# Kernel optimization log

Measured on AMD Instinct MI355X. Metric: run time of the kernel, lower is better.

## Reference

```python
import jax, jax.numpy as jnp
import numpy as np

N = 4096          # batch of candidate observations
D = 1024          # embedding dim
N_CLASSES = 100
GTG_MAX_ITER = 30 # gtg_tol=0.0 -> while loop always runs max_iter steps
PERC_LABELED = 0.5
EPS = 1e-8        # matches the +1e-08 in sum_X_A_X


def setup_inputs() -> dict:
    key = jax.random.key(0)
    k1, k2 = jax.random.split(key)
    embedding = jax.random.normal(k1, (N, D), dtype=jnp.float32)
    labels = jax.random.randint(k2, (N,), 0, N_CLASSES, dtype=jnp.int32)
    return {"embedding": embedding, "labels": labels}


def _cos_affinity(E):
    # F.normalize(E, dim=-1) with eps=1e-12, then relu(En @ En.T), diag := 1
    En = E / jnp.maximum(jnp.linalg.norm(E, axis=-1, keepdims=True), 1e-12)
    A = jax.nn.relu(En @ En.T)                      # [N, N]
    n = A.shape[0]
    idx = jnp.arange(n)
    A = A.at[idx, idx].set(1.0)
    return A, En


def reference(embedding, labels):
    n = embedding.shape[0]

    # ---- get_A_rbfk (A_function='cos_sim', rbf_aff=True) ----
    A, En = _cos_affinity(embedding)
    # 7th neighbor by descending cosine similarity (column index 6)
    idx7 = jnp.argsort(-A, axis=1)[:, 6]            # [N]
    # sigma_i = relu(cos(x_i, seventh_i)) -- the [0,1] entry of the 2x2 cos-sim matrix
    sigmas = jax.nn.relu(jnp.sum(En * En[idx7], axis=-1))  # [N]
    A = jnp.exp(-(A ** 2) / (sigmas[:, None] * sigmas[None, :]))

    # ---- threshold (strategy='mean', cos_sim branch) ----
    A = jnp.where(A < jnp.mean(A), 0.0, A)

    # ---- get_X: first n_lab indices labeled (one-hot), rest uniform 1/C ----
    n_lab = int(n * PERC_LABELED)
    labeled = jnp.arange(n) < n_lab                 # [N] bool
    one_hot = jax.nn.one_hot(labels, N_CLASSES, dtype=jnp.float32)
    X0 = jnp.where(labeled[:, None], one_hot, jnp.float32(1.0 / N_CLASSES))

    # ---- graph transduction game: X <- (X + X*(A@X)) / rowsum ----
    def step(X, _):
        mm_A_X = A @ X                              # [N, C]
        mult = X + X * mm_A_X
        Xn = mult / (jnp.sum(mult, axis=1, keepdims=True) + EPS)
        ent = -jnp.sum(Xn * jnp.log(Xn + EPS), axis=1)  # per-row entropy history
        return Xn, ent

    Xf, _ent_hist = jax.lax.scan(step, X0, None, length=GTG_MAX_ITER)
    return Xf
```

## Files before the change

### kernel.cpp

```cpp
#include <hip/hip_runtime.h>
#include <math.h>

typedef unsigned short ushortT;
typedef __attribute__((ext_vector_type(8))) short short8;
typedef __attribute__((ext_vector_type(4))) float f32x4;

#define NN 4096
#define DD 1024
#define NC 100
#define CP 128
#define NLAB 2048
#define NITER 30

__device__ __forceinline__ ushortT bf16rn(float x) {
  unsigned u = __float_as_uint(x);
  unsigned r = (u + 0x7fffu + ((u >> 16) & 1u)) >> 16;
  return (ushortT)r;
}
__device__ __forceinline__ float bf2f(ushortT h) {
  return __uint_as_float(((unsigned)h) << 16);
}
__device__ __forceinline__ void gload16(const void* g, void* l) {
  __builtin_amdgcn_global_load_lds((const __attribute__((address_space(1))) char*)g,
                                   (__attribute__((address_space(3))) char*)l, 16, 0, 0);
}

__global__ __launch_bounds__(256) void k_normalize(const float* __restrict__ E,
                                                   ushortT* __restrict__ Enh,
                                                   ushortT* __restrict__ Enl) {
  int row = blockIdx.x, t = threadIdx.x;
  const float4* e4 = (const float4*)(E + (size_t)row * DD);
  float4 v = e4[t];
  float ss = v.x * v.x + v.y * v.y + v.z * v.z + v.w * v.w;
  __shared__ float red[4];
  int lane = t & 63, w = t >> 6;
#pragma unroll
  for (int off = 32; off; off >>= 1) ss += __shfl_xor(ss, off);
  if (lane == 0) red[w] = ss;
  __syncthreads();
  float tot = red[0] + red[1] + red[2] + red[3];
  float d = fmaxf(sqrtf(tot), 1e-12f);
  float xs[4] = {v.x / d, v.y / d, v.z / d, v.w / d};
  ushort4 hv, lv;
  ushortT h;
  h = bf16rn(xs[0]); hv.x = h; lv.x = bf16rn(xs[0] - bf2f(h));
  h = bf16rn(xs[1]); hv.y = h; lv.y = bf16rn(xs[1] - bf2f(h));
  h = bf16rn(xs[2]); hv.z = h; lv.z = bf16rn(xs[2] - bf2f(h));
  h = bf16rn(xs[3]); hv.w = h; lv.w = bf16rn(xs[3] - bf2f(h));
  ((ushort4*)Enh)[(size_t)row * 256 + t] = hv;
  ((ushort4*)Enl)[(size_t)row * 256 + t] = lv;
}

__global__ __launch_bounds__(256, 4) void k_syrk_mfma(const ushortT* __restrict__ Enh,
                                                      const ushortT* __restrict__ Enl,
                                                      float* __restrict__ A) {
  int xg = (int)blockIdx.x & 7;
  int j = (int)blockIdx.x >> 3;
  int bi = -1, bj = 0;
#pragma unroll
  for (int p = 0; p < 4; ++p) {
    int bic = xg + (p << 3);
    int c = 32 - bic;
    if (bi < 0) {
      if (j < c) { bi = bic; bj = bic + j; } else j -= c;
    }
  }
  if (bi < 0) return;
  __shared__ ushortT lds[18432];
  int t = threadIdx.x;
  int l = t & 63, w = t >> 6;
  int i0 = bi << 7, j0 = bj << 7;
  int wr = w >> 1, wc = w & 1;
  f32x4 zz = {0.f, 0.f, 0.f, 0.f};
  f32x4 acc[4][4];
#pragma unroll
  for (int m = 0; m < 4; ++m)
#pragma unroll
    for (int n = 0; n < 4; ++n) acc[m][n] = zz;
  int arow_l = l & 15, kslot = l >> 4;

  for (int s = 0; s < 48; ++s) {
    int term = s >> 4;
    int kk0 = (s & 15) << 6;
    const ushortT* sa = (term == 2) ? Enl : Enh;
    const ushortT* sb = (term == 1) ? Enl : Enh;
#pragma unroll
    for (int q = 0; q < 4; ++q) {
      int n = (q << 8) + t;
      int r = n >> 3, p = n & 7;
      int col = (p ^ (r & 7)) << 3;
      gload16(sa + (size_t)(i0 + r) * DD + kk0 + col, &lds[n << 3]);
      gload16(sb + (size_t)(j0 + r) * DD + kk0 + col, &lds[8192 + (n << 3)]);
    }
    __syncthreads();
#pragma unroll
    for (int kk = 0; kk < 2; ++kk) {
      int g = (kk << 2) + kslot;
      short8 av[4], bv[4];
#pragma unroll
      for (int m = 0; m < 4; ++m) {
        int r = (wr << 6) + (m << 4) + arow_l;
        av[m] = *(const short8*)&lds[(r << 6) + ((g ^ (r & 7)) << 3)];
      }
#pragma unroll
      for (int n = 0; n < 4; ++n) {
        int r = (wc << 6) + (n << 4) + arow_l;
        bv[n] = *(const short8*)&lds[8192 + (r << 6) + ((g ^ (r & 7)) << 3)];
      }
#pragma unroll
      for (int m = 0; m < 4; ++m)
#pragma unroll
        for (int n = 0; n < 4; ++n)
          acc[m][n] = __builtin_amdgcn_mfma_f32_16x16x32_bf16(av[m], bv[n], acc[m][n], 0, 0, 0);
    }
    __syncthreads();
  }
  int rbase = (l >> 4) << 2;
#pragma unroll
  for (int m = 0; m < 4; ++m) {
#pragma unroll
    for (int n = 0; n < 4; ++n) {
#pragma unroll
      for (int r = 0; r < 4; ++r) {
        int gi = i0 + (wr << 6) + (m << 4) + rbase + r;
        int gj = j0 + (wc << 6) + (n << 4) + (l & 15);
        float v = fmaxf(acc[m][n][r], 0.0f);
        if (gi == gj) v = 1.0f;
        A[(size_t)gi * NN + gj] = v;
      }
    }
  }
  if (bi != bj) {
    float* T = (float*)&lds[0];
#pragma unroll
    for (int c2 = 0; c2 < 2; ++c2) {
      __syncthreads();
      if (wr == c2) {
#pragma unroll
        for (int m = 0; m < 4; ++m)
#pragma unroll
          for (int n = 0; n < 4; ++n)
#pragma unroll
            for (int r = 0; r < 4; ++r)
              T[(((wc << 6) + (n << 4) + (l & 15)) * 68) + (m << 4) + rbase + r] =
                  fmaxf(acc[m][n][r], 0.0f);
      }
      __syncthreads();
      int lj = t >> 1, cg = (t & 1) << 5;
#pragma unroll
      for (int q = 0; q < 8; ++q) {
        float4 vq = *(const float4*)&T[lj * 68 + cg + (q << 2)];
        *(float4*)&A[(size_t)(j0 + lj) * NN + i0 + (c2 << 6) + cg + (q << 2)] = vq;
      }
    }
  }
}

__device__ __forceinline__ void ins7(float (&tv)[7], float v) {
  if (v > tv[6]) {
#pragma unroll
    for (int s = 0; s < 7; s++) {
      if (v > tv[s]) { float tmp = tv[s]; tv[s] = v; v = tmp; }
    }
  }
}
__global__ __launch_bounds__(256) void k_top7(const float* __restrict__ A,
                                              float* __restrict__ sig) {
  int w = threadIdx.x >> 6, lane = threadIdx.x & 63;
  int row = (blockIdx.x << 2) + w;
  const float4* a4 = (const float4*)(A + (size_t)row * NN);
  float tv[7];
#pragma unroll
  for (int i = 0; i < 7; i++) tv[i] = -1.0f;
  for (int k = 0; k < 16; k++) {
    float4 v = a4[(k << 6) + lane];
    ins7(tv, v.x); ins7(tv, v.y); ins7(tv, v.z); ins7(tv, v.w);
  }
  int head = 0;
  float seventh = 0.0f;
  for (int r = 0; r < 7; r++) {
    float h = (head < 7) ? tv[head] : -1.0f;
    float m = h;
#pragma unroll
    for (int off = 32; off; off >>= 1) m = fmaxf(m, __shfl_xor(m, off));
    unsigned long long ball = __ballot(h == m);
    if (lane == (__ffsll(ball) - 1)) head++;
    seventh = m;
  }
  if (lane == 0) sig[row] = seventh;
}

__global__ __launch_bounds__(256) void k_transform(const float* __restrict__ A,
                                                   const float* __restrict__ sig,
                                                   double* __restrict__ parts) {
  int row = blockIdx.x;
  float si = sig[row];
  const float4* a4 = (const float4*)(A + (size_t)row * NN);
  const float4* s4 = (const float4*)sig;
  int t = threadIdx.x;
  double local = 0.0;
#pragma unroll
  for (int k = 0; k < 4; k++) {
    int j = (k << 8) + t;
    float4 v = a4[j];
    float4 sg = s4[j];
    local += (double)expf(-(v.x * v.x) / (si * sg.x)) +
             (double)expf(-(v.y * v.y) / (si * sg.y)) +
             (double)expf(-(v.z * v.z) / (si * sg.z)) +
             (double)expf(-(v.w * v.w) / (si * sg.w));
  }
  __shared__ double dred[4];
  int lane = t & 63, wv = t >> 6;
#pragma unroll
  for (int off = 32; off; off >>= 1) local += __shfl_xor(local, off);
  if (lane == 0) dred[wv] = local;
  __syncthreads();
  if (t == 0) parts[row] = dred[0] + dred[1] + dred[2] + dred[3];
}

__global__ __launch_bounds__(256) void k_mean(const double* __restrict__ parts,
                                              float* __restrict__ meanb) {
  int t = threadIdx.x;
  double local = 0.0;
#pragma unroll
  for (int k = 0; k < NN / 256; k++) local += parts[(k << 8) + t];
  __shared__ double dred[4];
  int lane = t & 63, wv = t >> 6;
#pragma unroll
  for (int off = 32; off; off >>= 1) local += __shfl_xor(local, off);
  if (lane == 0) dred[wv] = local;
  __syncthreads();
  if (t == 0) meanb[0] = (float)((dred[0] + dred[1] + dred[2] + dred[3]) / ((double)NN * (double)NN));
}

__global__ __launch_bounds__(256) void k_thresh_pack(const float* __restrict__ A,
                                                     const float* __restrict__ sig,
                                                     const float* __restrict__ meanb,
                                                     ushortT* __restrict__ ApL,
                                                     ushortT* __restrict__ ApU) {
  float m = meanb[0];
  int i4 = ((int)blockIdx.x << 8) + threadIdx.x;
  int row2 = i4 >> 10;
  int col4 = (i4 & 1023) << 2;
  int grow = NLAB + row2;
  float si = sig[grow];
  float4 v = *(const float4*)&A[(size_t)grow * NN + col4];
  float4 sg = *(const float4*)&sig[col4];
  float c0 = expf(-(v.x * v.x) / (si * sg.x));
  float c1 = expf(-(v.y * v.y) / (si * sg.y));
  float c2 = expf(-(v.z * v.z) / (si * sg.z));
  float c3 = expf(-(v.w * v.w) / (si * sg.w));
  c0 = (c0 < m) ? 0.0f : c0;
  c1 = (c1 < m) ? 0.0f : c1;
  c2 = (c2 < m) ? 0.0f : c2;
  c3 = (c3 < m) ? 0.0f : c3;
  int half = col4 >> 11;
  int cc = col4 & 2047;
  int rt = row2 >> 4, arow = row2 & 15;
  int kc = cc >> 5, khi = (cc >> 3) & 3, k0 = cc & 7;
  ushortT* dst = half ? ApU : ApL;
  ushort4 hv;
  hv.x = bf16rn(c0); hv.y = bf16rn(c1); hv.z = bf16rn(c2); hv.w = bf16rn(c3);
  *(ushort4*)&dst[((size_t)((rt << 6) + kc) << 9) + (khi << 7) + (arow << 3) + k0] = hv;
}

__global__ __launch_bounds__(256) void k_xlabp(const int* __restrict__ labels,
                                               ushortT* __restrict__ Xlabp) {
  int idx = ((int)blockIdx.x << 8) + threadIdx.x;
  int c = idx >> 11, j = idx & 2047;
  int kc = j >> 5, khi = (j >> 3) & 3, k0 = j & 7;
  int cf = c >> 4, slot = c & 15;
  Xlabp[((size_t)(((kc << 3) + cf) << 2) + khi) * 128 + (slot << 3) + k0] =
      (labels[j] == c) ? (ushortT)0x3F80 : (ushortT)0;
}

__global__ __launch_bounds__(64) void k_xinit(float* __restrict__ Xf,
                                              ushortT* __restrict__ Xp) {
  int rt = blockIdx.x, l = threadIdx.x;
  int col = l & 15, rg4 = l >> 4;
  int kc = rt >> 1;
  int kk = ((rt & 1) << 4) + (rg4 << 2);
  int khi = kk >> 3, k0 = kk & 7;
#pragma unroll
  for (int cf = 0; cf < 8; ++cf) {
    int cls = (cf << 4) + col;
    float v = (cls < NC) ? 0.01f : 0.0f;
    ((f32x4*)Xf)[(size_t)((rt << 3) + cf) * 64 + l] = (f32x4){v, v, v, v};
    ushortT h = bf16rn(v);
    ushort4 hv = {h, h, h, h};
    *(ushort4*)&Xp[((size_t)(((kc << 3) + cf) << 2) + khi) * 128 + (col << 3) + k0] = hv;
  }
}

__global__ __launch_bounds__(256) void k_gP(const ushortT* __restrict__ Ap,
                                            const ushortT* __restrict__ Xp,
                                            float* __restrict__ Pp) {
  int t = threadIdx.x, l = t & 63, w = t >> 6;
  int bid = (int)blockIdx.x;
  int rt = ((bid & 7) << 4) + ((bid >> 3) & 15);
  int s = bid >> 7;
  int kc0 = (s << 4) + (w << 2);
  const ushortT* ab = Ap + ((size_t)rt << 15) + ((size_t)kc0 << 9) + (l << 3);
  const ushortT* xb = Xp + ((size_t)kc0 << 12) + (l << 3);
  short8 av[4];
#pragma unroll
  for (int i = 0; i < 4; ++i) av[i] = *(const short8*)(ab + ((size_t)i << 9));
  f32x4 acc[8];
#pragma unroll
  for (int cf = 0; cf < 8; ++cf) {
    acc[cf] = (f32x4){0.f, 0.f, 0.f, 0.f};
#pragma unroll
    for (int i = 0; i < 4; ++i) {
      short8 bv = *(const short8*)(xb + ((size_t)i << 12) + (cf << 9));
      acc[cf] = __builtin_amdgcn_mfma_f32_16x16x32_bf16(av[i], bv, acc[cf], 0, 0, 0);
    }
  }
  __shared__ float red[4][8][64][4];
#pragma unroll
  for (int cf = 0; cf < 8; ++cf) *(f32x4*)&red[w][cf][l][0] = acc[cf];
  __syncthreads();
  if (w < 2) {
#pragma unroll
    for (int q = 0; q < 4; ++q) {
      int cf = (w << 2) + q;
      f32x4 sum = *(const f32x4*)&red[0][cf][l][0];
#pragma unroll
      for (int wp = 1; wp < 4; ++wp) {
        f32x4 p = *(const f32x4*)&red[wp][cf][l][0];
        sum[0] += p[0]; sum[1] += p[1]; sum[2] += p[2]; sum[3] += p[3];
      }
      ((f32x4*)Pp)[((size_t)(((s << 7) + rt) << 3) + cf) * 64 + l] = sum;
    }
  }
}

template <bool UPDATE>
__global__ __launch_bounds__(64) void k_updU(const float* __restrict__ Pp,
                                             const float* __restrict__ YlabF,
                                             const float* __restrict__ XfPrev,
                                             float* __restrict__ XfOut,
                                             ushortT* __restrict__ XpOut) {
  int rt = blockIdx.x, l = threadIdx.x;
  f32x4 acc[8];
#pragma unroll
  for (int cf = 0; cf < 8; ++cf) acc[cf] = (f32x4){0.f, 0.f, 0.f, 0.f};
  const f32x4* pq = (const f32x4*)Pp;
#pragma unroll
  for (int s = 0; s < 4; ++s) {
#pragma unroll
    for (int cf = 0; cf < 8; ++cf) {
      f32x4 p = pq[((size_t)(((s << 7) + rt) << 3) + cf) * 64 + l];
      acc[cf][0] += p[0]; acc[cf][1] += p[1];
      acc[cf][2] += p[2]; acc[cf][3] += p[3];
    }
  }
  if constexpr (!UPDATE) {
#pragma unroll
    for (int cf = 0; cf < 8; ++cf)
      ((f32x4*)XfOut)[(size_t)((rt << 3) + cf) * 64 + l] = acc[cf];
  } else {
    f32x4 mult[8];
    f32x4 rs = {0.f, 0.f, 0.f, 0.f};
#pragma unroll
    for (int cf = 0; cf < 8; ++cf) {
      f32x4 yl = ((const f32x4*)YlabF)[(size_t)((rt << 3) + cf) * 64 + l];
      f32x4 xv = ((const f32x4*)XfPrev)[(size_t)((rt << 3) + cf) * 64 + l];
#pragma unroll
      for (int r = 0; r < 4; ++r) {
        mult[cf][r] = fmaf(xv[r], acc[cf][r] + yl[r], xv[r]);
        rs[r] += mult[cf][r];
      }
    }
#pragma unroll
    for (int msk = 1; msk < 16; msk <<= 1) {
#pragma unroll
      for (int r = 0; r < 4; ++r) rs[r] += __shfl_xor(rs[r], msk);
    }
    f32x4 dn;
#pragma unroll
    for (int r = 0; r < 4; ++r) dn[r] = rs[r] + 1e-8f;
    int col = l & 15, rg4 = l >> 4;
    int kc = rt >> 1;
    int kk = ((rt & 1) << 4) + (rg4 << 2);
    int khi = kk >> 3, k0 = kk & 7;
#pragma unroll
    for (int cf = 0; cf < 8; ++cf) {
      f32x4 ov;
#pragma unroll
      for (int r = 0; r < 4; ++r) ov[r] = mult[cf][r] / dn[r];
      ((f32x4*)XfOut)[(size_t)((rt << 3) + cf) * 64 + l] = ov;
      ushort4 xo;
      xo.x = bf16rn(ov[0]); xo.y = bf16rn(ov[1]);
      xo.z = bf16rn(ov[2]); xo.w = bf16rn(ov[3]);
      *(ushort4*)&XpOut[((size_t)(((kc << 3) + cf) << 2) + khi) * 128 + (col << 3) + k0] = xo;
    }
  }
}

__global__ __launch_bounds__(256) void k_output(const float* __restrict__ Xf,
                                                const int* __restrict__ labels,
                                                float* __restrict__ out) {
  int idx = ((int)blockIdx.x << 8) + threadIdx.x;
  int i = idx / NC, c = idx - i * NC;
  float v;
  if (i < NLAB) {
    v = (labels[i] == c) ? 1.0f : 0.0f;
  } else {
    int row = i - NLAB;
    int rt = row >> 4, r = row & 15;
    int rg4 = r >> 2, reg = r & 3;
    int cf = c >> 4, col = c & 15;
    v = Xf[((size_t)(((rt << 3) + cf) << 6) + (rg4 << 4) + col) * 4 + reg];
  }
  out[idx] = v;
}

extern "C" void kernel_launch(void* const* d_in, const int* in_sizes, int n_in,
                              void* d_out, int out_size, void* d_ws, size_t ws_size,
                              hipStream_t stream) {
  const float* E = (const float*)d_in[0];
  const int* labels = (const int*)d_in[1];
  float* out = (float*)d_out;
  char* ws = (char*)d_ws;
  const size_t MB = 1024 * 1024;

  float* A = (float*)ws;
  ushortT* Enh = (ushortT*)(ws + 64 * MB);
  ushortT* Enl = (ushortT*)(ws + 72 * MB);
  ushortT* ApL = (ushortT*)(ws + 80 * MB);
  ushortT* ApU = (ushortT*)(ws + 88 * MB);
  float* sig = (float*)(ws + 96 * MB);
  double* parts = (double*)(ws + 96 * MB + 65536);
  float* meanb = (float*)(ws + 96 * MB + 131072);
  ushortT* Xlabp = (ushortT*)(ws + 97 * MB);
  float* YlabF = (float*)(ws + 98 * MB);
  float* Xf0 = (float*)(ws + 99 * MB);
  float* Xf1 = (float*)(ws + 100 * MB);
  ushortT* Xp0 = (ushortT*)(ws + 101 * MB);
  ushortT* Xp1 = (ushortT*)(ws + 102 * MB);
  float* Pp = (float*)(ws + 104 * MB);

  k_normalize<<<NN, 256, 0, stream>>>(E, Enh, Enl);
  k_syrk_mfma<<<640, 256, 0, stream>>>(Enh, Enl, A);
  k_top7<<<NN / 4, 256, 0, stream>>>(A, sig);
  k_transform<<<NN, 256, 0, stream>>>(A, sig, parts);
  k_mean<<<1, 256, 0, stream>>>(parts, meanb);
  k_thresh_pack<<<8192, 256, 0, stream>>>(A, sig, meanb, ApL, ApU);
  k_xlabp<<<1024, 256, 0, stream>>>(labels, Xlabp);
  k_xinit<<<128, 64, 0, stream>>>(Xf0, Xp0);
  k_gP<<<512, 256, 0, stream>>>(ApL, Xlabp, Pp);
  k_updU<false><<<128, 64, 0, stream>>>(Pp, nullptr, nullptr, YlabF, nullptr);
  float* xf[2] = {Xf0, Xf1};
  ushortT* xp[2] = {Xp0, Xp1};
  int cur = 0;
  for (int it = 0; it < NITER; ++it) {
    int nxt = cur ^ 1;
    k_gP<<<512, 256, 0, stream>>>(ApU, xp[cur], Pp);
    k_updU<true><<<128, 64, 0, stream>>>(Pp, YlabF, xf[cur], xf[nxt], xp[nxt]);
    cur = nxt;
  }
  k_output<<<1600, 256, 0, stream>>>(xf[cur], labels, out);
}
```

Measured before the change: 511.0 us.

## Fuse GTG matmul and row-normalize update into one kernel per iteration

Replaces the per-iteration pair of kernels (split-K partial matmul writing to a scratch buffer, then a reduce-and-update kernel) with a single kernel. Each block computes a full 16-row, 4-class-fragment slice with an in-block K reduction through LDS. The two class-halves of a row tile combine their row sums through global atomics and a spin-wait counter. This removes one launch and the partial-sum round trip per iteration, at the cost of an inter-block spin dependency that assumes both paired blocks are co-resident, and fewer, larger blocks.

```diff
diff --git a/kernel.cpp b/kernel.cpp
--- a/kernel.cpp
+++ b/kernel.cpp
@@ -334,67 +334,103 @@
   }
 }
 
-template <bool UPDATE>
-__global__ __launch_bounds__(64) void k_updU(const float* __restrict__ Pp,
-                                             const float* __restrict__ YlabF,
-                                             const float* __restrict__ XfPrev,
-                                             float* __restrict__ XfOut,
-                                             ushortT* __restrict__ XpOut) {
+__global__ __launch_bounds__(64) void k_updY(const float* __restrict__ Pp,
+                                             float* __restrict__ YlabF) {
   int rt = blockIdx.x, l = threadIdx.x;
-  f32x4 acc[8];
-#pragma unroll
-  for (int cf = 0; cf < 8; ++cf) acc[cf] = (f32x4){0.f, 0.f, 0.f, 0.f};
-  const f32x4* pq = (const f32x4*)Pp;
-#pragma unroll
-  for (int s = 0; s < 4; ++s) {
-#pragma unroll
-    for (int cf = 0; cf < 8; ++cf) {
-      f32x4 p = pq[((size_t)(((s << 7) + rt) << 3) + cf) * 64 + l];
-      acc[cf][0] += p[0]; acc[cf][1] += p[1];
-      acc[cf][2] += p[2]; acc[cf][3] += p[3];
-    }
-  }
-  if constexpr (!UPDATE) {
-#pragma unroll
-    for (int cf = 0; cf < 8; ++cf)
-      ((f32x4*)XfOut)[(size_t)((rt << 3) + cf) * 64 + l] = acc[cf];
-  } else {
-    f32x4 mult[8];
-    f32x4 rs = {0.f, 0.f, 0.f, 0.f};
-#pragma unroll
-    for (int cf = 0; cf < 8; ++cf) {
-      f32x4 yl = ((const f32x4*)YlabF)[(size_t)((rt << 3) + cf) * 64 + l];
-      f32x4 xv = ((const f32x4*)XfPrev)[(size_t)((rt << 3) + cf) * 64 + l];
-#pragma unroll
-      for (int r = 0; r < 4; ++r) {
-        mult[cf][r] = fmaf(xv[r], acc[cf][r] + yl[r], xv[r]);
-        rs[r] += mult[cf][r];
-      }
-    }
-#pragma unroll
-    for (int msk = 1; msk < 16; msk <<= 1) {
-#pragma unroll
-      for (int r = 0; r < 4; ++r) rs[r] += __shfl_xor(rs[r], msk);
-    }
-    f32x4 dn;
-#pragma unroll
-    for (int r = 0; r < 4; ++r) dn[r] = rs[r] + 1e-8f;
-    int col = l & 15, rg4 = l >> 4;
-    int kc = rt >> 1;
-    int kk = ((rt & 1) << 4) + (rg4 << 2);
-    int khi = kk >> 3, k0 = kk & 7;
-#pragma unroll
-    for (int cf = 0; cf < 8; ++cf) {
-      f32x4 ov;
-#pragma unroll
-      for (int r = 0; r < 4; ++r) ov[r] = mult[cf][r] / dn[r];
-      ((f32x4*)XfOut)[(size_t)((rt << 3) + cf) * 64 + l] = ov;
-      ushort4 xo;
-      xo.x = bf16rn(ov[0]); xo.y = bf16rn(ov[1]);
-      xo.z = bf16rn(ov[2]); xo.w = bf16rn(ov[3]);
-      *(ushort4*)&XpOut[((size_t)(((kc << 3) + cf) << 2) + khi) * 128 + (col << 3) + k0] = xo;
-    }
-  }
+#pragma unroll
+  for (int cf = 0; cf < 8; ++cf) {
+    f32x4 acc = (f32x4){0.f, 0.f, 0.f, 0.f};
+#pragma unroll
+    for (int s = 0; s < 4; ++s) {
+      f32x4 p = ((const f32x4*)Pp)[((size_t)(((s << 7) + rt) << 3) + cf) * 64 + l];
+      acc[0] += p[0]; acc[1] += p[1]; acc[2] += p[2]; acc[3] += p[3];
+    }
+    ((f32x4*)YlabF)[(size_t)((rt << 3) + cf) * 64 + l] = acc;
+  }
+}
+
+__global__ __launch_bounds__(256) void k_it2(
+    const ushortT* __restrict__ Ap,
+    const ushortT* __restrict__ Xp,
+    const float* __restrict__ YlabF, const float* __restrict__ XfPrev,
+    float* __restrict__ XfOut, ushortT* __restrict__ XpOut,
+    float* __restrict__ sums2,
+    int* __restrict__ cnt2) {
+  __shared__ float red[4][4][64][4];
+  __shared__ float sums_l[4][16];
+  __shared__ float totl[16];
+  int t = threadIdx.x, l = t & 63, w = t >> 6;
+  int bid = (int)blockIdx.x;
+  int rt = ((bid & 7) << 4) + ((bid >> 3) & 15);
+  int half = bid >> 7;
+  int cf = (half << 2) + w;
+
+  const ushortT* ab = Ap + ((size_t)rt << 15) + ((size_t)(w << 4) << 9) + (l << 3);
+  const ushortT* xb = Xp + ((size_t)(w << 4) << 12) + ((size_t)(half << 2) << 9) + (l << 3);
+  f32x4 acc[4];
+#pragma unroll
+  for (int cc = 0; cc < 4; ++cc) acc[cc] = (f32x4){0.f, 0.f, 0.f, 0.f};
+#pragma unroll
+  for (int i = 0; i < 16; ++i) {
+    short8 av = *(const short8*)(ab + ((size_t)i << 9));
+#pragma unroll
+    for (int cc = 0; cc < 4; ++cc) {
+      short8 bv = *(const short8*)(xb + ((size_t)i << 12) + (cc << 9));
+      acc[cc] = __builtin_amdgcn_mfma_f32_16x16x32_bf16(av, bv, acc[cc], 0, 0, 0);
+    }
+  }
+#pragma unroll
+  for (int cc = 0; cc < 4; ++cc) *(f32x4*)&red[w][cc][l][0] = acc[cc];
+  __syncthreads();
+  f32x4 mm = (f32x4){0.f, 0.f, 0.f, 0.f};
+#pragma unroll
+  for (int wp = 0; wp < 4; ++wp) {
+    f32x4 p = *(const f32x4*)&red[wp][w][l][0];
+    mm[0] += p[0]; mm[1] += p[1]; mm[2] += p[2]; mm[3] += p[3];
+  }
+  size_t fo = (size_t)((rt << 3) + cf) * 64 + l;
+  f32x4 yl = ((const f32x4*)YlabF)[fo];
+  f32x4 xv = ((const f32x4*)XfPrev)[fo];
+  f32x4 mult, rs;
+#pragma unroll
+  for (int r = 0; r < 4; ++r) {
+    mult[r] = fmaf(xv[r], mm[r] + yl[r], xv[r]);
+    rs[r] = mult[r];
+  }
+#pragma unroll
+  for (int msk = 1; msk < 16; msk <<= 1) {
+#pragma unroll
+    for (int r = 0; r < 4; ++r) rs[r] += __shfl_xor(rs[r], msk);
+  }
+  int rg4 = l >> 4, col16 = l & 15;
+  if (col16 == 0) {
+#pragma unroll
+    for (int r = 0; r < 4; ++r) sums_l[w][(rg4 << 2) + r] = rs[r];
+  }
+  __syncthreads();
+  if (w == 0 && l < 16) {
+    float hs = sums_l[0][l] + sums_l[1][l] + sums_l[2][l] + sums_l[3][l];
+    atomicAdd(&sums2[(rt << 4) + l], hs);
+  }
+  if (t == 0) {
+    asm volatile("s_waitcnt vmcnt(0)" ::: "memory");
+    atomicAdd(&cnt2[rt], 1);
+    while (atomicAdd(&cnt2[rt], 0) < 2) __builtin_amdgcn_s_sleep(2);
+  }
+  __syncthreads();
+  if (w == 0 && l < 16) totl[l] = atomicAdd(&sums2[(rt << 4) + l], 0.0f) + 1e-8f;
+  __syncthreads();
+  f32x4 ov;
+#pragma unroll
+  for (int r = 0; r < 4; ++r) ov[r] = mult[r] / totl[(rg4 << 2) + r];
+  ((f32x4*)XfOut)[fo] = ov;
+  int kcp = rt >> 1;
+  int rem = ((rt & 1) << 4) + (rg4 << 2);
+  int khi = rem >> 3, k0 = rem & 7;
+  ushort4 xo;
+  xo.x = bf16rn(ov[0]); xo.y = bf16rn(ov[1]);
+  xo.z = bf16rn(ov[2]); xo.w = bf16rn(ov[3]);
+  *(ushort4*)&XpOut[((size_t)(((kcp << 3) + cf) << 2) + khi) * 128 + (col16 << 3) + k0] = xo;
 }
 
 __global__ __launch_bounds__(256) void k_output(const float* __restrict__ Xf,
@@ -439,6 +475,8 @@
   ushortT* Xp0 = (ushortT*)(ws + 101 * MB);
   ushortT* Xp1 = (ushortT*)(ws + 102 * MB);
   float* Pp = (float*)(ws + 104 * MB);
+  float* sums2 = (float*)(ws + 108 * MB);
+  int* cnt2 = (int*)(ws + 109 * MB);
 
   k_normalize<<<NN, 256, 0, stream>>>(E, Enh, Enl);
   k_syrk_mfma<<<640, 256, 0, stream>>>(Enh, Enl, A);
@@ -448,15 +486,17 @@
   k_thresh_pack<<<8192, 256, 0, stream>>>(A, sig, meanb, ApL, ApU);
   k_xlabp<<<1024, 256, 0, stream>>>(labels, Xlabp);
   k_xinit<<<128, 64, 0, stream>>>(Xf0, Xp0);
+  hipMemsetAsync(sums2, 0, (size_t)NITER * 128 * 16 * sizeof(float), stream);
+  hipMemsetAsync(cnt2, 0, (size_t)NITER * 128 * sizeof(int), stream);
   k_gP<<<512, 256, 0, stream>>>(ApL, Xlabp, Pp);
-  k_updU<false><<<128, 64, 0, stream>>>(Pp, nullptr, nullptr, YlabF, nullptr);
+  k_updY<<<128, 64, 0, stream>>>(Pp, YlabF);
   float* xf[2] = {Xf0, Xf1};
   ushortT* xp[2] = {Xp0, Xp1};
   int cur = 0;
   for (int it = 0; it < NITER; ++it) {
     int nxt = cur ^ 1;
-    k_gP<<<512, 256, 0, stream>>>(ApU, xp[cur], Pp);
-    k_updU<true><<<128, 64, 0, stream>>>(Pp, YlabF, xf[cur], xf[nxt], xp[nxt]);
+    k_it2<<<256, 256, 0, stream>>>(ApU, xp[cur], YlabF, xf[cur], xf[nxt], xp[nxt],
+                                   sums2 + (size_t)it * 2048, cnt2 + (size_t)it * 128);
     cur = nxt;
   }
   k_output<<<1600, 256, 0, stream>>>(xf[cur], labels, out);
```

Measured after the change: 478.4 us. 1.07x faster.
